# Kernel optimization log

Hardware: AMD Instinct MI355X
Metric: run time of the kernel (lower is better)

Reference implementation:

```python
import jax, jax.numpy as jnp
import numpy as np

B, P, M, N, H, K, EH = 16, 50, 512, 1024, 64, 20, 200


def setup_inputs() -> dict:
    key = jax.random.key(0)
    ks = jax.random.split(key, 16)
    b = jax.random.normal(ks[0], (B, P, M, 1), jnp.float32)
    A = jax.random.normal(ks[1], (1, P, M, N), jnp.float32) / np.float32(np.sqrt(M))
    # random undirected multigraph on P nodes, stored with both directions
    s = jax.random.randint(ks[2], (B, EH), 0, P)
    off = jax.random.randint(ks[3], (B, EH), 1, P)
    d = (s + off) % P
    edge_index = jnp.stack([jnp.concatenate([s, d], 1), jnp.concatenate([d, s], 1)], 1).astype(jnp.int32)  # [B,2,2*EH]

    def lin(k, fi, fo, scale=None):
        scale = np.float32(1.0 / np.sqrt(fi)) if scale is None else np.float32(scale)
        return jax.random.normal(k, (fi, fo), jnp.float32) * scale, jnp.zeros((fo,), jnp.float32)

    W_e1, b_e1 = lin(ks[4], P * M, P * H)
    W_e2, b_e2 = lin(ks[5], P * H, 2 * P * H)
    W_e3, b_e3 = lin(ks[6], 2 * P * H, 4 * P * H)
    W_c1, b_c1 = lin(ks[7], 4 * H, 2 * H)
    W_c2, b_c2 = lin(ks[8], 2 * H, 2 * H)
    W_f1, b_f1 = lin(ks[9], 2 * H, H)
    W_f2, _ = lin(ks[10], H, K * 4, scale=1e-3)
    b_f2 = jnp.full((K * 4,), -2.0, jnp.float32)  # mimics fc2 init (tiny weights, negative bias)
    max_param = jnp.array([0.01, 0.1, 0.1, 0.1], jnp.float32).reshape(1, 1, 1, 4)  # [alpha,tau,rho,eta]_max
    y0 = jax.random.normal(ks[11], (B, P, N, 1), jnp.float32) * 0.01
    u0 = jax.random.normal(ks[12], (B, P, N, 1), jnp.float32) * 0.01
    d0 = jax.random.normal(ks[13], (B, P, N, 1), jnp.float32) * 0.01
    return dict(b=b, A=A, edge_index=edge_index, max_param=max_param,
                W_e1=W_e1, b_e1=b_e1, W_e2=W_e2, b_e2=b_e2, W_e3=W_e3, b_e3=b_e3,
                W_c1=W_c1, b_c1=b_c1, W_c2=W_c2, b_c2=b_c2,
                W_f1=W_f1, b_f1=b_f1, W_f2=W_f2, b_f2=b_f2,
                y0=y0, u0=u0, d0=d0)


def _lrelu(x):
    return jax.nn.leaky_relu(x, 0.01)


def _gcn(x, s, d, W, bias):
    # GCNConv: sym-normalized propagation with self loops. x: [P,F]
    h = x @ W
    deg = jnp.zeros((x.shape[0],), x.dtype).at[d].add(1.0) + 1.0  # +1 self loop
    dinv = jax.lax.rsqrt(deg)
    agg = jnp.zeros_like(h).at[d].add(h[s] * (dinv[s] * dinv[d])[:, None])
    agg = agg + h * (dinv * dinv)[:, None]  # self-loop term
    return agg + bias


def _delta(y, s, d):
    # nested neighbor loop: for each directed edge (s,d): delta[s]+=y[s]-y[d]; delta[d]-=same
    diff = y[s] - y[d]  # [E,N,1]
    return jnp.zeros_like(y).at[s].add(diff).at[d].add(-diff)


def reference(b, A, edge_index, max_param,
              W_e1, b_e1, W_e2, b_e2, W_e3, b_e3,
              W_c1, b_c1, W_c2, b_c2, W_f1, b_f1, W_f2, b_f2,
              y0, u0, d0):
    Bb = b.shape[0]
    n = A.shape[3]
    k_steps = W_f2.shape[1] // 4
    src, dst = edge_index[:, 0], edge_index[:, 1]

    # ---- GNN hypernetwork ----
    x = b.reshape(Bb, -1)
    x = _lrelu(x @ W_e1 + b_e1)
    x = _lrelu(x @ W_e2 + b_e2)
    x = (x @ W_e3 + b_e3).reshape(Bb, P, -1)  # [B,P,4H]
    x = _lrelu(jax.vmap(lambda xf, s, d: _gcn(xf, s, d, W_c1, b_c1))(x, src, dst))
    x = _lrelu(jax.vmap(lambda xf, s, d: _gcn(xf, s, d, W_c2, b_c2))(x, src, dst))
    x = x.mean(axis=1)  # global_mean_pool over nodes
    x = _lrelu(x @ W_f1 + b_f1)
    hyp = (x @ W_f2 + b_f2).reshape(Bb, k_steps, 1, 4)
    hyp = jax.nn.sigmoid(jnp.cumsum(hyp, axis=1)) * max_param  # [B,K,1,4]
    hyp_scan = jnp.transpose(hyp, (1, 3, 0, 2))[..., None, None]  # [K,4,B,1,1,1]

    # ---- precompute ----
    A0 = A[0]  # [P,M,N]
    AtA = jnp.einsum('pmn,pmk->pnk', A0, A0)  # [P,N,N]
    Atb = jnp.einsum('pmn,bpmo->bpno', A0, b)  # [B,P,N,1]
    sum_nb = jax.vmap(lambda s: jnp.zeros((P,), b.dtype).at[s].add(1.0))(src)[:, :, None, None]  # [B,P,1,1]

    # ---- unrolled D-ADMM / DLASSO ----
    def step(carry, hk):
        y_k, U_k, dlt = carry
        alpha, tau, rho, eta = hk[0], hk[1], hk[2], hk[3]
        AtAy = jnp.einsum('pnk,bpko->bpno', AtA, y_k)
        g = AtAy - Atb + jnp.sign(y_k) * tau + U_k * sum_nb + dlt * rho
        y_n = y_k - alpha * g
        dlt_n = jax.vmap(_delta)(y_n, src, dst)
        U_n = U_k + dlt_n * eta
        return (y_n, U_n, dlt_n), y_n

    _, Y = jax.lax.scan(step, (y0, u0, d0), hyp_scan)
    return Y  # [K,B,P,N,1]
```

## Files before the change

### kernel.cpp

```cpp
#include <hip/hip_runtime.h>

namespace {
constexpr int NB = 16;
constexpr int NP = 50;
constexpr int NM = 512;
constexpr int NN = 1024;
constexpr int NK = 20;
constexpr long ASZ = (long)NP * NM * NN;
constexpr long YSZ = (long)NB * NP * NN;
}

typedef __attribute__((ext_vector_type(8))) short bf16x8;
typedef __attribute__((ext_vector_type(4))) float f32x4;

__device__ __forceinline__ float lrelu(float x){ return x > 0.f ? x : 0.01f*x; }
__device__ __forceinline__ unsigned short f2bf(float f){
  unsigned u = __builtin_bit_cast(unsigned, f);
  u += 0x7fffu + ((u >> 16) & 1u);
  return (unsigned short)(u >> 16);
}

__global__ __launch_bounds__(256) void k_prep(const float* __restrict__ A,
                      unsigned short* __restrict__ abfT){
  const int p = blockIdx.x, mt = blockIdx.y, nt = blockIdx.z;
  const int tid = threadIdx.x;
  __shared__ unsigned short tile[64][72];
  const int m0 = mt*64, n0 = nt*64;
  {
    int r = tid>>2, cs = (tid&3)*16;
    const float* src = A + ((long)p*NM + m0 + r)*NN + n0 + cs;
    unsigned short tmp[16];
    #pragma unroll
    for (int q=0;q<16;q+=4){
      float4 v = *(const float4*)(src+q);
      tmp[q+0]=f2bf(v.x); tmp[q+1]=f2bf(v.y); tmp[q+2]=f2bf(v.z); tmp[q+3]=f2bf(v.w);
    }
    #pragma unroll
    for (int q=0;q<16;q++) tile[r][cs+q] = tmp[q];
  }
  __syncthreads();
  {
    int r = tid>>2, cs = (tid&3)*16;
    unsigned short* dst = abfT + ((long)p*NN + n0 + r)*NM + m0 + cs;
    unsigned short tmp[16];
    #pragma unroll
    for (int q=0;q<16;q++) tmp[q] = tile[cs+q][r];
    #pragma unroll
    for (int q=0;q<16;q+=8) *(uint4*)(dst+q) = *(const uint4*)&tmp[q];
  }
}

__global__ void k_init(const float* __restrict__ y0, const float* __restrict__ u0,
                       const float* __restrict__ d0, float* __restrict__ y,
                       float* __restrict__ u, float* __restrict__ dl,
                       unsigned short* __restrict__ ybf, int n){
  int e = (blockIdx.x*blockDim.x + threadIdx.x)*4;
  if (e >= n) return;
  float4 a = *(const float4*)(y0+e);
  *(float4*)(y+e) = a;
  ushort4 o; o.x=f2bf(a.x); o.y=f2bf(a.y); o.z=f2bf(a.z); o.w=f2bf(a.w);
  *(ushort4*)(ybf+e) = o;
  *(float4*)(u+e)  = *(const float4*)(u0+e);
  *(float4*)(dl+e) = *(const float4*)(d0+e);
}

__global__ __launch_bounds__(256) void k_atb(const unsigned short* __restrict__ abfT,
                      const float* __restrict__ src, float* __restrict__ z){
  const int p = blockIdx.x;
  const int tid = threadIdx.x, wave = tid>>6, lane = tid&63;
  __shared__ unsigned short tlds[16][520];
  {
    int b = tid>>4, c0 = (tid&15)*8;
    const float* tr = src + ((long)b*NP + p)*NM;
    #pragma unroll
    for (int it=0; it<4; it++){
      float4 lo = *(const float4*)(tr + it*128 + c0);
      float4 hi = *(const float4*)(tr + it*128 + c0 + 4);
      unsigned short w[8];
      w[0]=f2bf(lo.x); w[1]=f2bf(lo.y); w[2]=f2bf(lo.z); w[3]=f2bf(lo.w);
      w[4]=f2bf(hi.x); w[5]=f2bf(hi.y); w[6]=f2bf(hi.z); w[7]=f2bf(hi.w);
      *(uint4*)&tlds[b][it*128 + c0] = *(const uint4*)w;
    }
  }
  __syncthreads();
  const int lr = lane&15, kg = lane>>4;
  const int nt0 = blockIdx.y*4 + wave;
  const int n0 = nt0*16, n1 = (nt0+32)*16;
  const unsigned short* b0 = abfT + ((long)p*NN + n0 + lr)*NM + kg*8;
  const unsigned short* b1 = abfT + ((long)p*NN + n1 + lr)*NM + kg*8;
  const unsigned short* tp = &tlds[lr][kg*8];
  f32x4 acc0a={0.f,0.f,0.f,0.f}, acc0b={0.f,0.f,0.f,0.f};
  f32x4 acc1a={0.f,0.f,0.f,0.f}, acc1b={0.f,0.f,0.f,0.f};
  #pragma unroll 4
  for (int ks=0; ks<16; ks+=2){
    bf16x8 t0 = *(const bf16x8*)(tp + ks*32);
    bf16x8 t1 = *(const bf16x8*)(tp + ks*32 + 32);
    bf16x8 b00 = *(const bf16x8*)(b0 + (long)ks*32);
    bf16x8 b01 = *(const bf16x8*)(b0 + (long)ks*32 + 32);
    bf16x8 b10 = *(const bf16x8*)(b1 + (long)ks*32);
    bf16x8 b11 = *(const bf16x8*)(b1 + (long)ks*32 + 32);
    acc0a = __builtin_amdgcn_mfma_f32_16x16x32_bf16(t0, b00, acc0a, 0, 0, 0);
    acc1a = __builtin_amdgcn_mfma_f32_16x16x32_bf16(t0, b10, acc1a, 0, 0, 0);
    acc0b = __builtin_amdgcn_mfma_f32_16x16x32_bf16(t1, b01, acc0b, 0, 0, 0);
    acc1b = __builtin_amdgcn_mfma_f32_16x16x32_bf16(t1, b11, acc1b, 0, 0, 0);
  }
  f32x4 acc0 = acc0a + acc0b;
  f32x4 acc1 = acc1a + acc1b;
  #pragma unroll
  for (int r=0;r<4;r++){
    int bb = kg*4 + r;
    z[((long)bb*NP + p)*NN + n0 + lr] = acc0[r];
    z[((long)bb*NP + p)*NN + n1 + lr] = acc1[r];
  }
}

__global__ __launch_bounds__(256) void k_ata(const unsigned short* __restrict__ abfT,
                      unsigned short* __restrict__ ata){
  const int p = blockIdx.x;
  int yy = blockIdx.y, bi = 0;
  while (yy >= 8 - bi){ yy -= 8 - bi; bi++; }
  const int bj = bi + yy;
  const int i0 = bi*128, j0 = bj*128;
  const int tid = threadIdx.x, wave = tid>>6, lane = tid&63;
  const int lr = lane&15, kg = lane>>4;
  __shared__ unsigned short pa[128][72];
  __shared__ unsigned short pb[128][72];
  f32x4 acc[2][8];
  #pragma unroll
  for (int ti=0;ti<2;ti++)
    #pragma unroll
    for (int tj=0;tj<8;tj++) acc[ti][tj] = (f32x4){0.f,0.f,0.f,0.f};
  const unsigned short* Abase = abfT + (long)p*NN*NM;
  for (int mc=0; mc<NM; mc+=64){
    __syncthreads();
    {
      int r = tid>>1, c0 = (tid&1)*32;
      const unsigned short* sa = Abase + (long)(i0 + r)*NM + mc + c0;
      const unsigned short* sb = Abase + (long)(j0 + r)*NM + mc + c0;
      #pragma unroll
      for (int q=0;q<32;q+=8){
        *(uint4*)&pa[r][c0+q] = *(const uint4*)(sa+q);
        *(uint4*)&pb[r][c0+q] = *(const uint4*)(sb+q);
      }
    }
    __syncthreads();
    #pragma unroll
    for (int ks=0; ks<2; ks++){
      bf16x8 av0 = *(const bf16x8*)&pa[wave*32      + lr][ks*32 + kg*8];
      bf16x8 av1 = *(const bf16x8*)&pa[wave*32 + 16 + lr][ks*32 + kg*8];
      #pragma unroll
      for (int tj=0;tj<8;tj++){
        bf16x8 bv = *(const bf16x8*)&pb[tj*16 + lr][ks*32 + kg*8];
        acc[0][tj] = __builtin_amdgcn_mfma_f32_16x16x32_bf16(av0, bv, acc[0][tj], 0,0,0);
        acc[1][tj] = __builtin_amdgcn_mfma_f32_16x16x32_bf16(av1, bv, acc[1][tj], 0,0,0);
      }
    }
  }
  const long pbase = (long)p << 20;
  #pragma unroll
  for (int ti=0; ti<2; ti++){
    const int ib = i0 + wave*32 + ti*16;
    #pragma unroll
    for (int tj=0; tj<8; tj++){
      const int jb = j0 + tj*16;
      unsigned short w[4];
      #pragma unroll
      for (int r=0;r<4;r++) w[r] = f2bf(acc[ti][tj][r]);
      #pragma unroll
      for (int r=0;r<4;r++)
        ata[pbase + (long)(ib + kg*4 + r)*1024 + jb + lr] = w[r];
      if (bi != bj)
        *(ushort4*)(ata + pbase + (long)(jb + lr)*1024 + ib + kg*4) = *(const ushort4*)w;
    }
  }
}

__global__ __launch_bounds__(256) void k_enc2(const float* __restrict__ X, const float* __restrict__ W,
                           float* __restrict__ part, int fi, int fo, int ichunk, int actin){
  const int tid = threadIdx.x;
  const int o0 = (blockIdx.x*256 + tid)*4;
  const int c  = blockIdx.y;
  const bool ok = o0 < fo;
  __shared__ float xs[64][16];
  float4 acc[16];
  #pragma unroll
  for (int b=0;b<16;b++){ acc[b].x=0.f; acc[b].y=0.f; acc[b].z=0.f; acc[b].w=0.f; }
  const long ibase = (long)c*ichunk;
  const int xb = tid&15, xio = (tid>>4)*4;
  for (int s=0; s<ichunk; s+=64){
    float4 v = *(const float4*)(X + (long)xb*fi + ibase + s + xio);
    if (actin){ v.x=lrelu(v.x); v.y=lrelu(v.y); v.z=lrelu(v.z); v.w=lrelu(v.w); }
    __syncthreads();
    xs[xio+0][xb]=v.x; xs[xio+1][xb]=v.y; xs[xio+2][xb]=v.z; xs[xio+3][xb]=v.w;
    __syncthreads();
    const float* wp = W + (ibase+s)*fo + o0;
    #pragma unroll 4
    for (int i=0;i<64;i++){
      float4 w;
      if (ok) w = *(const float4*)(wp + (long)i*fo);
      else { w.x=0.f; w.y=0.f; w.z=0.f; w.w=0.f; }
      #pragma unroll
      for (int b2=0;b2<16;b2+=4){
        float4 x4 = *(const float4*)&xs[i][b2];
        acc[b2+0].x += w.x*x4.x; acc[b2+0].y += w.y*x4.x; acc[b2+0].z += w.z*x4.x; acc[b2+0].w += w.w*x4.x;
        acc[b2+1].x += w.x*x4.y; acc[b2+1].y += w.y*x4.y; acc[b2+1].z += w.z*x4.y; acc[b2+1].w += w.w*x4.y;
        acc[b2+2].x += w.x*x4.z; acc[b2+2].y += w.y*x4.z; acc[b2+2].z += w.z*x4.z; acc[b2+2].w += w.w*x4.z;
        acc[b2+3].x += w.x*x4.w; acc[b2+3].y += w.y*x4.w; acc[b2+3].z += w.z*x4.w; acc[b2+3].w += w.w*x4.w;
      }
    }
  }
  if (ok){
    float* pp = part + ((long)c*16)*fo + o0;
    #pragma unroll
    for (int b=0;b<16;b++) *(float4*)(pp + (long)b*fo) = acc[b];
  }
}

__global__ void k_enc_reduce(const float* __restrict__ part, const float* __restrict__ bias,
                             float* __restrict__ out, int fo, int nchunk){
  int i = blockIdx.x*256 + threadIdx.x;
  if (i >= 16*fo) return;
  int o = i % fo;
  float s = bias[o];
  for (int c=0;c<nchunk;c++) s += part[(long)c*16*fo + i];
  out[i] = s;
}

__global__ __launch_bounds__(64) void k_graph(const int* __restrict__ ei, float* __restrict__ adjg,
                        float* __restrict__ dmg, float* __restrict__ snbg){
  const int b = blockIdx.x, tid = threadIdx.x;
  __shared__ float adj[2500], dm[2500], deg[50], dinv[50], snb[50];
  for (int i=tid;i<2500;i+=64){ adj[i]=0.f; dm[i]=0.f; }
  if (tid<50){ deg[tid]=0.f; snb[tid]=0.f; }
  __syncthreads();
  const int* e = ei + b*800;
  for (int k=tid;k<400;k+=64){
    atomicAdd(&deg[e[400+k]], 1.f);
    atomicAdd(&snb[e[k]], 1.f);
  }
  __syncthreads();
  if (tid<50) dinv[tid] = 1.f / sqrtf(deg[tid] + 1.f);
  __syncthreads();
  for (int k=tid;k<400;k+=64){
    int s = e[k], d = e[400+k];
    atomicAdd(&adj[d*50+s], dinv[s]*dinv[d]);
    atomicAdd(&dm[s*50+s],  1.f); atomicAdd(&dm[s*50+d], -1.f);
    atomicAdd(&dm[d*50+d],  1.f); atomicAdd(&dm[d*50+s], -1.f);
  }
  __syncthreads();
  if (tid<50) adj[tid*50+tid] += dinv[tid]*dinv[tid];
  __syncthreads();
  for (int i=tid;i<2500;i+=64){ adjg[b*2500+i]=adj[i]; dmg[b*2500+i]=dm[i]; }
  if (tid<50) snbg[b*50+tid]=snb[tid];
}

__global__ __launch_bounds__(256) void k_gnn(const float* __restrict__ h3,
     const float* __restrict__ Wc1, const float* __restrict__ bc1,
     const float* __restrict__ Wc2, const float* __restrict__ bc2,
     const float* __restrict__ Wf1, const float* __restrict__ bf1,
     const float* __restrict__ Wf2, const float* __restrict__ bf2,
     const float* __restrict__ maxp, const float* __restrict__ adjg,
     float* __restrict__ hypg){
  const int b = blockIdx.x, tid = threadIdx.x;
  __shared__ float adj[2500];
  __shared__ float bufA[6400];
  __shared__ float bufB[6400];
  __shared__ float xm[128], hv1[64], raw[80];
  for (int i=tid;i<2500;i+=256) adj[i] = adjg[b*2500+i];

  const int j = tid & 127, nh = tid >> 7;
  float acc[25];
  #pragma unroll
  for (int q=0;q<25;q++) acc[q]=0.f;
  for (int ic=0; ic<4; ic++){
    __syncthreads();
    for (int e=tid; e<800; e+=256){
      int n = e>>4, seg = (e&15)*4;
      *(float4*)&bufB[n*64+seg] = *(const float4*)(h3 + (long)b*12800 + n*256 + ic*64 + seg);
    }
    __syncthreads();
    for (int i=0;i<64;i+=4){
      float w0 = Wc1[(long)(ic*64+i+0)*128 + j];
      float w1 = Wc1[(long)(ic*64+i+1)*128 + j];
      float w2 = Wc1[(long)(ic*64+i+2)*128 + j];
      float w3 = Wc1[(long)(ic*64+i+3)*128 + j];
      #pragma unroll
      for (int q=0;q<25;q++){
        float4 xv = *(const float4*)&bufB[(nh*25+q)*64 + i];
        acc[q] += xv.x*w0 + xv.y*w1 + xv.z*w2 + xv.w*w3;
      }
    }
  }
  __syncthreads();
  #pragma unroll
  for (int q=0;q<25;q++) bufA[(nh*25+q)*128 + j] = acc[q];
  __syncthreads();
  {
    float a2[25];
    float bv = bc1[j];
    #pragma unroll
    for (int q=0;q<25;q++) a2[q]=bv;
    for (int qq=0; qq<50; qq++){
      float hvv = bufA[qq*128 + j];
      #pragma unroll
      for (int q=0;q<25;q++) a2[q] += adj[(nh*25+q)*50 + qq]*hvv;
    }
    __syncthreads();
    #pragma unroll
    for (int q=0;q<25;q++) bufB[(nh*25+q)*128 + j] = lrelu(a2[q]);
  }
  __syncthreads();
  {
    float a2[25];
    #pragma unroll
    for (int q=0;q<25;q++) a2[q]=0.f;
    for (int i=0;i<128;i+=4){
      float w0 = Wc2[(long)(i+0)*128 + j];
      float w1 = Wc2[(long)(i+1)*128 + j];
      float w2 = Wc2[(long)(i+2)*128 + j];
      float w3 = Wc2[(long)(i+3)*128 + j];
      #pragma unroll
      for (int q=0;q<25;q++){
        float4 xv = *(const float4*)&bufB[(nh*25+q)*128 + i];
        a2[q] += xv.x*w0 + xv.y*w1 + xv.z*w2 + xv.w*w3;
      }
    }
    __syncthreads();
    #pragma unroll
    for (int q=0;q<25;q++) bufA[(nh*25+q)*128 + j] = a2[q];
  }
  __syncthreads();
  {
    float a2[25];
    float bv = bc2[j];
    #pragma unroll
    for (int q=0;q<25;q++) a2[q]=bv;
    for (int qq=0; qq<50; qq++){
      float hvv = bufA[qq*128 + j];
      #pragma unroll
      for (int q=0;q<25;q++) a2[q] += adj[(nh*25+q)*50 + qq]*hvv;
    }
    __syncthreads();
    #pragma unroll
    for (int q=0;q<25;q++) bufB[(nh*25+q)*128 + j] = lrelu(a2[q]);
  }
  __syncthreads();
  if (tid < 128){
    float s = 0.f;
    for (int n=0;n<50;n++) s += bufB[n*128 + tid];
    xm[tid] = s * (1.f/50.f);
  }
  __syncthreads();
  if (tid < 64){
    float s = bf1[tid];
    for (int i=0;i<128;i++) s += xm[i]*Wf1[i*64 + tid];
    hv1[tid] = lrelu(s);
  }
  __syncthreads();
  if (tid < 80){
    float s = bf2[tid];
    for (int i=0;i<64;i++) s += hv1[i]*Wf2[i*80 + tid];
    raw[tid] = s;
  }
  __syncthreads();
  if (tid < 4){
    float c = 0.f;
    for (int k=0;k<20;k++){
      c += raw[k*4 + tid];
      hypg[b*80 + k*4 + tid] = maxp[tid] / (1.f + expf(-c));
    }
  }
}

__global__ __launch_bounds__(256) void k_z(const unsigned short* __restrict__ ata,
      const unsigned short* __restrict__ ybin, const float* __restrict__ atb,
      const float* __restrict__ u, const float* __restrict__ dl,
      const float* __restrict__ snbg, const float* __restrict__ hypg, int k,
      float* __restrict__ y, unsigned short* __restrict__ ybout,
      float* __restrict__ yout){
  const int p = blockIdx.x;
  const int tid = threadIdx.x, wave = tid>>6, lane = tid&63;
  __shared__ unsigned short ylds[16][1032];
  {
    int b = tid>>4, c0 = (tid&15)*8;
    const unsigned short* yr = ybin + ((long)b*NP + p)*NN;
    #pragma unroll
    for (int it=0; it<8; it++)
      *(uint4*)&ylds[b][it*128 + c0] = *(const uint4*)(yr + it*128 + c0);
  }
  __syncthreads();
  const int lr = lane&15, kg = lane>>4;
  const int nt0 = blockIdx.y*4 + wave;
  const int n0 = nt0*16, n1 = n0 + 512;
  const long pb2 = (long)p << 20;
  const unsigned short* b0 = ata + pb2 + (long)(n0 + lr)*1024 + kg*8;
  const unsigned short* b1 = ata + pb2 + (long)(n1 + lr)*1024 + kg*8;
  const unsigned short* yp = &ylds[lr][kg*8];
  f32x4 acc0a={0.f,0.f,0.f,0.f}, acc0b={0.f,0.f,0.f,0.f};
  f32x4 acc1a={0.f,0.f,0.f,0.f}, acc1b={0.f,0.f,0.f,0.f};
  #pragma unroll 4
  for (int ks=0; ks<32; ks+=2){
    bf16x8 y0v = *(const bf16x8*)(yp + ks*32);
    bf16x8 y1v = *(const bf16x8*)(yp + ks*32 + 32);
    bf16x8 b00 = *(const bf16x8*)(b0 + ks*32);
    bf16x8 b01 = *(const bf16x8*)(b0 + ks*32 + 32);
    bf16x8 b10 = *(const bf16x8*)(b1 + ks*32);
    bf16x8 b11 = *(const bf16x8*)(b1 + ks*32 + 32);
    acc0a = __builtin_amdgcn_mfma_f32_16x16x32_bf16(y0v, b00, acc0a, 0,0,0);
    acc1a = __builtin_amdgcn_mfma_f32_16x16x32_bf16(y0v, b10, acc1a, 0,0,0);
    acc0b = __builtin_amdgcn_mfma_f32_16x16x32_bf16(y1v, b01, acc0b, 0,0,0);
    acc1b = __builtin_amdgcn_mfma_f32_16x16x32_bf16(y1v, b11, acc1b, 0,0,0);
  }
  f32x4 z0 = acc0a + acc0b;
  f32x4 z1 = acc1a + acc1b;
  #pragma unroll
  for (int r=0;r<4;r++){
    const int b = kg*4 + r;
    const float4 hp = *(const float4*)(hypg + b*80 + k*4);
    const float sp = snbg[b*NP + p];
    const long base = ((long)b*NP + p)*NN;
    {
      const long idx = base + n0 + lr;
      float yv = y[idx];
      float g = z0[r] - atb[idx] + ((yv>0.f)?1.f:((yv<0.f)?-1.f:0.f))*hp.y
              + u[idx]*sp + dl[idx]*hp.z;
      float ynv = yv - hp.x*g;
      y[idx] = ynv; ybout[idx] = f2bf(ynv); yout[(long)k*YSZ + idx] = ynv;
    }
    {
      const long idx = base + n1 + lr;
      float yv = y[idx];
      float g = z1[r] - atb[idx] + ((yv>0.f)?1.f:((yv<0.f)?-1.f:0.f))*hp.y
              + u[idx]*sp + dl[idx]*hp.z;
      float ynv = yv - hp.x*g;
      y[idx] = ynv; ybout[idx] = f2bf(ynv); yout[(long)k*YSZ + idx] = ynv;
    }
  }
}

__global__ __launch_bounds__(256) void k_dm(const float* __restrict__ dmg,
      const float* __restrict__ hypg, int k, const float* __restrict__ y,
      float* __restrict__ u, float* __restrict__ dl){
  const int b = blockIdx.x, n0 = blockIdx.y*128, tid = threadIdx.x;
  __shared__ float ys[50][128];
  __shared__ float dms[2500];
  for (int i=tid;i<2500;i+=256) dms[i] = dmg[b*2500+i];
  for (int e=tid; e<6400; e+=256){
    int p=e>>7, nn=e&127;
    ys[p][nn] = y[((long)b*NP+p)*NN + n0 + nn];
  }
  __syncthreads();
  const float eta = hypg[b*80 + k*4 + 3];
  for (int e=tid; e<6400; e+=256){
    int p=e>>7, nn=e&127;
    float s=0.f;
    #pragma unroll 10
    for (int q=0;q<NP;q++) s += dms[p*50+q]*ys[q][nn];
    long idx = ((long)b*NP+p)*NN + n0 + nn;
    dl[idx]=s;
    u[idx]+=s*eta;
  }
}

extern "C" void kernel_launch(void* const* d_in, const int* in_sizes, int n_in,
                              void* d_out, int out_size, void* d_ws, size_t ws_size,
                              hipStream_t stream){
  (void)in_sizes; (void)n_in; (void)out_size; (void)ws_size;
  const float* bin = (const float*)d_in[0];
  const float* A   = (const float*)d_in[1];
  const int*   ei  = (const int*)d_in[2];
  const float* mxp = (const float*)d_in[3];
  const float* We1 = (const float*)d_in[4];  const float* be1 = (const float*)d_in[5];
  const float* We2 = (const float*)d_in[6];  const float* be2 = (const float*)d_in[7];
  const float* We3 = (const float*)d_in[8];  const float* be3 = (const float*)d_in[9];
  const float* Wc1 = (const float*)d_in[10]; const float* bc1 = (const float*)d_in[11];
  const float* Wc2 = (const float*)d_in[12]; const float* bc2 = (const float*)d_in[13];
  const float* Wf1 = (const float*)d_in[14]; const float* bf1 = (const float*)d_in[15];
  const float* Wf2 = (const float*)d_in[16]; const float* bf2 = (const float*)d_in[17];
  const float* y0  = (const float*)d_in[18];
  const float* u0  = (const float*)d_in[19];
  const float* dd0 = (const float*)d_in[20];
  float* out = (float*)d_out;

  char* cur = (char*)d_ws;
  auto alloc = [&](size_t bytes)->void*{
    void* pp = (void*)cur; cur += (bytes + 255) & ~(size_t)255; return pp;
  };
  unsigned short* abfT = (unsigned short*)alloc(ASZ*2);
  unsigned short* ata  = (unsigned short*)alloc((size_t)NP*1024*1024*2);
  float* atb = (float*)alloc(YSZ*4);
  float* y   = (float*)alloc(YSZ*4);
  unsigned short* ybf0 = (unsigned short*)alloc(YSZ*2);
  unsigned short* ybf1 = (unsigned short*)alloc(YSZ*2);
  float* u   = (float*)alloc(YSZ*4);
  float* dl  = (float*)alloc(YSZ*4);
  float* h1  = (float*)alloc((size_t)16*3200*4);
  float* h2  = (float*)alloc((size_t)16*6400*4);
  float* h3  = (float*)alloc((size_t)16*12800*4);
  float* adj = (float*)alloc((size_t)16*2500*4);
  float* dm  = (float*)alloc((size_t)16*2500*4);
  float* snb = (float*)alloc((size_t)16*50*4);
  float* hyp = (float*)alloc((size_t)16*80*4);
  float* part= (float*)alloc((size_t)21000000);

  k_prep<<<dim3(50,8,16), dim3(256), 0, stream>>>(A, abfT);
  k_init<<<dim3(800), dim3(256), 0, stream>>>(y0, u0, dd0, y, u, dl, ybf0, (int)YSZ);
  k_atb<<<dim3(50,8), dim3(256), 0, stream>>>(abfT, bin, atb);
  k_ata<<<dim3(50,36), dim3(256), 0, stream>>>(abfT, ata);

  k_enc2<<<dim3(4,50),  dim3(256), 0, stream>>>(bin, We1, part, 25600, 3200, 512, 0);
  k_enc_reduce<<<dim3(200), dim3(256), 0, stream>>>(part, be1, h1, 3200, 50);
  k_enc2<<<dim3(7,25),  dim3(256), 0, stream>>>(h1, We2, part, 3200, 6400, 128, 1);
  k_enc_reduce<<<dim3(400), dim3(256), 0, stream>>>(part, be2, h2, 6400, 25);
  k_enc2<<<dim3(13,25), dim3(256), 0, stream>>>(h2, We3, part, 6400, 12800, 256, 1);
  k_enc_reduce<<<dim3(800), dim3(256), 0, stream>>>(part, be3, h3, 12800, 25);

  k_graph<<<dim3(16), dim3(64), 0, stream>>>(ei, adj, dm, snb);
  k_gnn<<<dim3(16), dim3(256), 0, stream>>>(h3, Wc1, bc1, Wc2, bc2, Wf1, bf1, Wf2, bf2, mxp, adj, hyp);

  for (int k=0;k<NK;k++){
    const unsigned short* ybin = (k & 1) ? ybf1 : ybf0;
    unsigned short* ybout      = (k & 1) ? ybf0 : ybf1;
    k_z <<<dim3(50,8), dim3(256), 0, stream>>>(ata, ybin, atb, u, dl, snb, hyp, k, y, ybout, out);
    k_dm<<<dim3(16,8), dim3(256), 0, stream>>>(dm, hyp, k, y, u, dl);
  }
}
```

Measured before the change: 1.514 ms.

## Precompute fused ADMM correction term and retile z kernel and encoder splits

```diff
diff --git a/kernel.cpp b/kernel.cpp
--- a/kernel.cpp
+++ b/kernel.cpp
@@ -51,8 +51,7 @@
 }
 
 __global__ void k_init(const float* __restrict__ y0, const float* __restrict__ u0,
-                       const float* __restrict__ d0, float* __restrict__ y,
-                       float* __restrict__ u, float* __restrict__ dl,
+                       float* __restrict__ y, float* __restrict__ u,
                        unsigned short* __restrict__ ybf, int n){
   int e = (blockIdx.x*blockDim.x + threadIdx.x)*4;
   if (e >= n) return;
@@ -61,7 +60,22 @@
   ushort4 o; o.x=f2bf(a.x); o.y=f2bf(a.y); o.z=f2bf(a.z); o.w=f2bf(a.w);
   *(ushort4*)(ybf+e) = o;
   *(float4*)(u+e)  = *(const float4*)(u0+e);
-  *(float4*)(dl+e) = *(const float4*)(d0+e);
+}
+
+__global__ __launch_bounds__(256) void k_c0(const float* __restrict__ u0,
+      const float* __restrict__ d0, const float* __restrict__ snbg,
+      const float* __restrict__ hypg, float* __restrict__ c){
+  long e = ((long)blockIdx.x*256 + threadIdx.x)*4;
+  if (e >= YSZ) return;
+  long bp = e >> 10;
+  int b = (int)(bp/NP), p = (int)(bp%NP);
+  float sp = snbg[b*NP+p], rho = hypg[b*80 + 2];
+  float4 uv = *(const float4*)(u0+e);
+  float4 dv = *(const float4*)(d0+e);
+  float4 cv;
+  cv.x = uv.x*sp + dv.x*rho; cv.y = uv.y*sp + dv.y*rho;
+  cv.z = uv.z*sp + dv.z*rho; cv.w = uv.w*sp + dv.w*rho;
+  *(float4*)(c+e) = cv;
 }
 
 __global__ __launch_bounds__(256) void k_atb(const unsigned short* __restrict__ abfT,
@@ -374,8 +388,7 @@
 
 __global__ __launch_bounds__(256) void k_z(const unsigned short* __restrict__ ata,
       const unsigned short* __restrict__ ybin, const float* __restrict__ atb,
-      const float* __restrict__ u, const float* __restrict__ dl,
-      const float* __restrict__ snbg, const float* __restrict__ hypg, int k,
+      const float* __restrict__ cbuf, const float* __restrict__ hypg, int k,
       float* __restrict__ y, unsigned short* __restrict__ ybout,
       float* __restrict__ yout){
   const int p = blockIdx.x;
@@ -388,59 +401,54 @@
     for (int it=0; it<8; it++)
       *(uint4*)&ylds[b][it*128 + c0] = *(const uint4*)(yr + it*128 + c0);
   }
-  __syncthreads();
   const int lr = lane&15, kg = lane>>4;
-  const int nt0 = blockIdx.y*4 + wave;
-  const int n0 = nt0*16, n1 = n0 + 512;
+  const int n0 = (blockIdx.y*4 + wave)*16;
   const long pb2 = (long)p << 20;
-  const unsigned short* b0 = ata + pb2 + (long)(n0 + lr)*1024 + kg*8;
-  const unsigned short* b1 = ata + pb2 + (long)(n1 + lr)*1024 + kg*8;
+  const unsigned short* bp = ata + pb2 + (long)(n0 + lr)*1024 + kg*8;
   const unsigned short* yp = &ylds[lr][kg*8];
-  f32x4 acc0a={0.f,0.f,0.f,0.f}, acc0b={0.f,0.f,0.f,0.f};
-  f32x4 acc1a={0.f,0.f,0.f,0.f}, acc1b={0.f,0.f,0.f,0.f};
-  #pragma unroll 4
-  for (int ks=0; ks<32; ks+=2){
-    bf16x8 y0v = *(const bf16x8*)(yp + ks*32);
-    bf16x8 y1v = *(const bf16x8*)(yp + ks*32 + 32);
-    bf16x8 b00 = *(const bf16x8*)(b0 + ks*32);
-    bf16x8 b01 = *(const bf16x8*)(b0 + ks*32 + 32);
-    bf16x8 b10 = *(const bf16x8*)(b1 + ks*32);
-    bf16x8 b11 = *(const bf16x8*)(b1 + ks*32 + 32);
-    acc0a = __builtin_amdgcn_mfma_f32_16x16x32_bf16(y0v, b00, acc0a, 0,0,0);
-    acc1a = __builtin_amdgcn_mfma_f32_16x16x32_bf16(y0v, b10, acc1a, 0,0,0);
-    acc0b = __builtin_amdgcn_mfma_f32_16x16x32_bf16(y1v, b01, acc0b, 0,0,0);
-    acc1b = __builtin_amdgcn_mfma_f32_16x16x32_bf16(y1v, b11, acc1b, 0,0,0);
-  }
-  f32x4 z0 = acc0a + acc0b;
-  f32x4 z1 = acc1a + acc1b;
+
+  float yv4[4], atb4[4], c4[4];
+  float4 hp4[4];
   #pragma unroll
   for (int r=0;r<4;r++){
     const int b = kg*4 + r;
-    const float4 hp = *(const float4*)(hypg + b*80 + k*4);
-    const float sp = snbg[b*NP + p];
-    const long base = ((long)b*NP + p)*NN;
-    {
-      const long idx = base + n0 + lr;
-      float yv = y[idx];
-      float g = z0[r] - atb[idx] + ((yv>0.f)?1.f:((yv<0.f)?-1.f:0.f))*hp.y
-              + u[idx]*sp + dl[idx]*hp.z;
-      float ynv = yv - hp.x*g;
-      y[idx] = ynv; ybout[idx] = f2bf(ynv); yout[(long)k*YSZ + idx] = ynv;
-    }
-    {
-      const long idx = base + n1 + lr;
-      float yv = y[idx];
-      float g = z1[r] - atb[idx] + ((yv>0.f)?1.f:((yv<0.f)?-1.f:0.f))*hp.y
-              + u[idx]*sp + dl[idx]*hp.z;
-      float ynv = yv - hp.x*g;
-      y[idx] = ynv; ybout[idx] = f2bf(ynv); yout[(long)k*YSZ + idx] = ynv;
-    }
+    const long idx = ((long)b*NP + p)*NN + n0 + lr;
+    yv4[r] = y[idx]; atb4[r] = atb[idx]; c4[r] = cbuf[idx];
+    hp4[r] = *(const float4*)(hypg + b*80 + k*4);
+  }
+  __syncthreads();
+
+  f32x4 a0={0.f,0.f,0.f,0.f}, a1={0.f,0.f,0.f,0.f}, a2={0.f,0.f,0.f,0.f}, a3={0.f,0.f,0.f,0.f};
+  #pragma unroll 4
+  for (int i=0;i<8;i++){
+    bf16x8 b0 = *(const bf16x8*)(bp + (i*4+0)*32);
+    bf16x8 b1 = *(const bf16x8*)(bp + (i*4+1)*32);
+    bf16x8 b2 = *(const bf16x8*)(bp + (i*4+2)*32);
+    bf16x8 b3 = *(const bf16x8*)(bp + (i*4+3)*32);
+    bf16x8 y0 = *(const bf16x8*)(yp + (i*4+0)*32);
+    bf16x8 y1 = *(const bf16x8*)(yp + (i*4+1)*32);
+    bf16x8 y2 = *(const bf16x8*)(yp + (i*4+2)*32);
+    bf16x8 y3 = *(const bf16x8*)(yp + (i*4+3)*32);
+    a0 = __builtin_amdgcn_mfma_f32_16x16x32_bf16(y0, b0, a0, 0,0,0);
+    a1 = __builtin_amdgcn_mfma_f32_16x16x32_bf16(y1, b1, a1, 0,0,0);
+    a2 = __builtin_amdgcn_mfma_f32_16x16x32_bf16(y2, b2, a2, 0,0,0);
+    a3 = __builtin_amdgcn_mfma_f32_16x16x32_bf16(y3, b3, a3, 0,0,0);
+  }
+  f32x4 z = (a0 + a1) + (a2 + a3);
+  #pragma unroll
+  for (int r=0;r<4;r++){
+    const int b = kg*4 + r;
+    const long idx = ((long)b*NP + p)*NN + n0 + lr;
+    float yv = yv4[r];
+    float g = z[r] - atb4[r] + ((yv>0.f)?1.f:((yv<0.f)?-1.f:0.f))*hp4[r].y + c4[r];
+    float ynv = yv - hp4[r].x*g;
+    y[idx] = ynv; ybout[idx] = f2bf(ynv); yout[(long)k*YSZ + idx] = ynv;
   }
 }
 
 __global__ __launch_bounds__(256) void k_dm(const float* __restrict__ dmg,
-      const float* __restrict__ hypg, int k, const float* __restrict__ y,
-      float* __restrict__ u, float* __restrict__ dl){
+      const float* __restrict__ snbg, const float* __restrict__ hypg, int k,
+      const float* __restrict__ y, float* __restrict__ u, float* __restrict__ c){
   const int b = blockIdx.x, n0 = blockIdx.y*128, tid = threadIdx.x;
   __shared__ float ys[50][128];
   __shared__ float dms[2500];
@@ -451,14 +459,16 @@
   }
   __syncthreads();
   const float eta = hypg[b*80 + k*4 + 3];
+  const float rhon = hypg[b*80 + (k+1)*4 + 2];
   for (int e=tid; e<6400; e+=256){
     int p=e>>7, nn=e&127;
     float s=0.f;
     #pragma unroll 10
     for (int q=0;q<NP;q++) s += dms[p*50+q]*ys[q][nn];
     long idx = ((long)b*NP+p)*NN + n0 + nn;
-    dl[idx]=s;
-    u[idx]+=s*eta;
+    float un = u[idx] + s*eta;
+    u[idx] = un;
+    c[idx] = un*snbg[b*NP+p] + s*rhon;
   }
 }
 
@@ -493,7 +503,7 @@
   unsigned short* ybf0 = (unsigned short*)alloc(YSZ*2);
   unsigned short* ybf1 = (unsigned short*)alloc(YSZ*2);
   float* u   = (float*)alloc(YSZ*4);
-  float* dl  = (float*)alloc(YSZ*4);
+  float* cb  = (float*)alloc(YSZ*4);
   float* h1  = (float*)alloc((size_t)16*3200*4);
   float* h2  = (float*)alloc((size_t)16*6400*4);
   float* h3  = (float*)alloc((size_t)16*12800*4);
@@ -501,27 +511,29 @@
   float* dm  = (float*)alloc((size_t)16*2500*4);
   float* snb = (float*)alloc((size_t)16*50*4);
   float* hyp = (float*)alloc((size_t)16*80*4);
-  float* part= (float*)alloc((size_t)21000000);
+  float* part= (float*)alloc((size_t)84000000);
 
   k_prep<<<dim3(50,8,16), dim3(256), 0, stream>>>(A, abfT);
-  k_init<<<dim3(800), dim3(256), 0, stream>>>(y0, u0, dd0, y, u, dl, ybf0, (int)YSZ);
+  k_init<<<dim3(800), dim3(256), 0, stream>>>(y0, u0, y, u, ybf0, (int)YSZ);
   k_atb<<<dim3(50,8), dim3(256), 0, stream>>>(abfT, bin, atb);
   k_ata<<<dim3(50,36), dim3(256), 0, stream>>>(abfT, ata);
 
-  k_enc2<<<dim3(4,50),  dim3(256), 0, stream>>>(bin, We1, part, 25600, 3200, 512, 0);
-  k_enc_reduce<<<dim3(200), dim3(256), 0, stream>>>(part, be1, h1, 3200, 50);
-  k_enc2<<<dim3(7,25),  dim3(256), 0, stream>>>(h1, We2, part, 3200, 6400, 128, 1);
-  k_enc_reduce<<<dim3(400), dim3(256), 0, stream>>>(part, be2, h2, 6400, 25);
-  k_enc2<<<dim3(13,25), dim3(256), 0, stream>>>(h2, We3, part, 6400, 12800, 256, 1);
-  k_enc_reduce<<<dim3(800), dim3(256), 0, stream>>>(part, be3, h3, 12800, 25);
+  k_enc2<<<dim3(4,200),  dim3(256), 0, stream>>>(bin, We1, part, 25600, 3200, 128, 0);
+  k_enc_reduce<<<dim3(200), dim3(256), 0, stream>>>(part, be1, h1, 3200, 200);
+  k_enc2<<<dim3(7,50),  dim3(256), 0, stream>>>(h1, We2, part, 3200, 6400, 64, 1);
+  k_enc_reduce<<<dim3(400), dim3(256), 0, stream>>>(part, be2, h2, 6400, 50);
+  k_enc2<<<dim3(13,100), dim3(256), 0, stream>>>(h2, We3, part, 6400, 12800, 64, 1);
+  k_enc_reduce<<<dim3(800), dim3(256), 0, stream>>>(part, be3, h3, 12800, 100);
 
   k_graph<<<dim3(16), dim3(64), 0, stream>>>(ei, adj, dm, snb);
   k_gnn<<<dim3(16), dim3(256), 0, stream>>>(h3, Wc1, bc1, Wc2, bc2, Wf1, bf1, Wf2, bf2, mxp, adj, hyp);
+  k_c0<<<dim3(800), dim3(256), 0, stream>>>(u0, dd0, snb, hyp, cb);
 
   for (int k=0;k<NK;k++){
     const unsigned short* ybin = (k & 1) ? ybf1 : ybf0;
     unsigned short* ybout      = (k & 1) ? ybf0 : ybf1;
-    k_z <<<dim3(50,8), dim3(256), 0, stream>>>(ata, ybin, atb, u, dl, snb, hyp, k, y, ybout, out);
-    k_dm<<<dim3(16,8), dim3(256), 0, stream>>>(dm, hyp, k, y, u, dl);
-  }
-}
+    k_z<<<dim3(50,16), dim3(256), 0, stream>>>(ata, ybin, atb, cb, hyp, k, y, ybout, out);
+    if (k < NK-1)
+      k_dm<<<dim3(16,8), dim3(256), 0, stream>>>(dm, snb, hyp, k, y, u, cb);
+  }
+}
```

After: 1.530 ms. Within noise of the previous version (+1.1%).
